# Performance work log

Measured on AMD Instinct MI355X. Metric: run time of the kernel, lower is better.

Reference implementation:

```python
import jax, jax.numpy as jnp
import numpy as np

MANTISSA_BITS = 3  # from init_kwargs


def _bfp_quantize(x, mantissa_bits):
    """Block floating-point quantization.

    Block = the channel vector at each (n, h, w) location (axis=1 of NCHW).
    Shared exponent e is that of the block's max |value| (frexp convention:
    max_abs = m * 2^e with m in [0.5, 1)), so max_abs/2^e in [0.5, 1).
    Each element keeps `mantissa_bits` mantissa bits relative to the shared
    exponent; extra bits are truncated (toward zero), matching mantissa
    right-shift + truncation in the reference CPU/CUDA kernels.
    """
    max_abs = jnp.max(jnp.abs(x), axis=1, keepdims=True)  # [N,1,H,W]
    _, e = jnp.frexp(max_abs)                              # shared exponent per block
    delta = jnp.exp2((e - mantissa_bits).astype(x.dtype))  # quantization step
    q = jnp.trunc(x / delta) * delta
    # zero blocks quantize to zero (trunc(0)=0 already, but be explicit)
    return jnp.where(max_abs > 0, q, jnp.zeros_like(x))


def setup_inputs() -> dict:
    key = jax.random.key(0)
    activations = jax.random.normal(key, (64, 256, 56, 56), dtype=jnp.float32)
    return {"activations": activations}


def reference(activations):
    return _bfp_quantize(activations, MANTISSA_BITS)
```

## Files before the change

kernel.cpp:

```cpp
#include <hip/hip_runtime.h>
#include <cstdint>


constexpr int C     = 256;
constexpr int HW    = 56 * 56;
constexpr int HW4   = HW / 4;
constexpr int CHW4  = C * HW4;
constexpr int CHUNK = 16;

__device__ __forceinline__ int fexp(float x) {
    int e;
    (void)frexpf(x, &e);
    return e;
}

__global__ __launch_bounds__(256, 4)
void bfp_kernel(const float4* __restrict__ in, float4* __restrict__ out, int total4) {
    int tid  = blockIdx.x * 256 + threadIdx.x;
    int wave = tid >> 6;
    int lane = threadIdx.x & 63;
    int s    = wave * 4 + (lane & 3);
    if (s >= total4) return;
    int k    = lane >> 2;

    int n  = s / HW4;
    int s4 = s - n * HW4;

    const float4* p = in  + (size_t)n * CHW4 + (size_t)k * CHUNK * HW4 + s4;
    float4*       q = out + (size_t)n * CHW4 + (size_t)k * CHUNK * HW4 + s4;

    float4 v[CHUNK];
#pragma unroll
    for (int i = 0; i < CHUNK; ++i) v[i] = p[i * HW4];

    float4 m = make_float4(0.f, 0.f, 0.f, 0.f);
#pragma unroll
    for (int i = 0; i < CHUNK; ++i) {
        m.x = fmaxf(m.x, fabsf(v[i].x));
        m.y = fmaxf(m.y, fabsf(v[i].y));
        m.z = fmaxf(m.z, fabsf(v[i].z));
        m.w = fmaxf(m.w, fabsf(v[i].w));
    }

#pragma unroll
    for (int mask = 4; mask < 64; mask <<= 1) {
        m.x = fmaxf(m.x, __shfl_xor(m.x, mask));
        m.y = fmaxf(m.y, __shfl_xor(m.y, mask));
        m.z = fmaxf(m.z, __shfl_xor(m.z, mask));
        m.w = fmaxf(m.w, __shfl_xor(m.w, mask));
    }

    int ex = fexp(m.x), ey = fexp(m.y), ez = fexp(m.z), ew = fexp(m.w);
    float dx = ldexpf(1.f, ex - 3), ix = ldexpf(1.f, 3 - ex);
    float dy = ldexpf(1.f, ey - 3), iy = ldexpf(1.f, 3 - ey);
    float dz = ldexpf(1.f, ez - 3), iz = ldexpf(1.f, 3 - ez);
    float dw = ldexpf(1.f, ew - 3), iw = ldexpf(1.f, 3 - ew);

#pragma unroll
    for (int i = 0; i < CHUNK; ++i) {
        float4 r;
        r.x = truncf(v[i].x * ix) * dx;
        r.y = truncf(v[i].y * iy) * dy;
        r.z = truncf(v[i].z * iz) * dz;
        r.w = truncf(v[i].w * iw) * dw;
        q[i * HW4] = r;
    }
}

extern "C" void kernel_launch(void* const* d_in, const int* in_sizes, int n_in,
                              void* d_out, int out_size, void* d_ws, size_t ws_size,
                              hipStream_t stream) {
    const float* in = (const float*)d_in[0];
    float* out      = (float*)d_out;
    int N      = in_sizes[0] / (C * HW);
    int total4 = N * HW4;
    int waves  = (total4 + 3) / 4;
    int blocks = (waves + 3) / 4;
    bfp_kernel<<<blocks, 256, 0, stream>>>((const float4*)in, (float4*)out, total4);
}
```

Before: 92.51 us.

## Re-read inputs instead of holding in registers, raise occupancy, use nontemporal stores

```diff
diff --git a/kernel.cpp b/kernel.cpp
--- a/kernel.cpp
+++ b/kernel.cpp
@@ -8,13 +8,22 @@
 constexpr int CHW4  = C * HW4;
 constexpr int CHUNK = 16;
 
+typedef float vfloat4 __attribute__((ext_vector_type(4)));
+
 __device__ __forceinline__ int fexp(float x) {
     int e;
     (void)frexpf(x, &e);
     return e;
 }
 
-__global__ __launch_bounds__(256, 4)
+__device__ __forceinline__ void fmax4(float4& m, const float4& v) {
+    m.x = fmaxf(m.x, fabsf(v.x));
+    m.y = fmaxf(m.y, fabsf(v.y));
+    m.z = fmaxf(m.z, fabsf(v.z));
+    m.w = fmaxf(m.w, fabsf(v.w));
+}
+
+__global__ __launch_bounds__(256, 8)
 void bfp_kernel(const float4* __restrict__ in, float4* __restrict__ out, int total4) {
     int tid  = blockIdx.x * 256 + threadIdx.x;
     int wave = tid >> 6;
@@ -29,18 +38,20 @@
     const float4* p = in  + (size_t)n * CHW4 + (size_t)k * CHUNK * HW4 + s4;
     float4*       q = out + (size_t)n * CHW4 + (size_t)k * CHUNK * HW4 + s4;
 
-    float4 v[CHUNK];
+    float4 m0 = make_float4(0.f, 0.f, 0.f, 0.f), m1 = m0, m2 = m0, m3 = m0;
 #pragma unroll
-    for (int i = 0; i < CHUNK; ++i) v[i] = p[i * HW4];
-
-    float4 m = make_float4(0.f, 0.f, 0.f, 0.f);
-#pragma unroll
-    for (int i = 0; i < CHUNK; ++i) {
-        m.x = fmaxf(m.x, fabsf(v[i].x));
-        m.y = fmaxf(m.y, fabsf(v[i].y));
-        m.z = fmaxf(m.z, fabsf(v[i].z));
-        m.w = fmaxf(m.w, fabsf(v[i].w));
+    for (int i = 0; i < CHUNK; i += 4) {
+        float4 a = p[(i + 0) * HW4];
+        float4 b = p[(i + 1) * HW4];
+        float4 c = p[(i + 2) * HW4];
+        float4 d = p[(i + 3) * HW4];
+        fmax4(m0, a); fmax4(m1, b); fmax4(m2, c); fmax4(m3, d);
     }
+    float4 m;
+    m.x = fmaxf(fmaxf(m0.x, m1.x), fmaxf(m2.x, m3.x));
+    m.y = fmaxf(fmaxf(m0.y, m1.y), fmaxf(m2.y, m3.y));
+    m.z = fmaxf(fmaxf(m0.z, m1.z), fmaxf(m2.z, m3.z));
+    m.w = fmaxf(fmaxf(m0.w, m1.w), fmaxf(m2.w, m3.w));
 
 #pragma unroll
     for (int mask = 4; mask < 64; mask <<= 1) {
@@ -58,12 +69,13 @@
 
 #pragma unroll
     for (int i = 0; i < CHUNK; ++i) {
-        float4 r;
-        r.x = truncf(v[i].x * ix) * dx;
-        r.y = truncf(v[i].y * iy) * dy;
-        r.z = truncf(v[i].z * iz) * dz;
-        r.w = truncf(v[i].w * iw) * dw;
-        q[i * HW4] = r;
+        float4 v = p[i * HW4];
+        vfloat4 r;
+        r.x = truncf(v.x * ix) * dx;
+        r.y = truncf(v.y * iy) * dy;
+        r.z = truncf(v.z * iz) * dz;
+        r.w = truncf(v.w * iw) * dw;
+        __builtin_nontemporal_store(r, (vfloat4*)&q[i * HW4]);
     }
 }
 
```

New measurement: 272.0 us. +194.0%, slower.
